# Performance work log

Hardware: AMD Instinct MI355X
Metric: run time of the kernel (lower is better)

## Reference

```python
import jax, jax.numpy as jnp
import numpy as np

N, T, GX, GY, GQ = 16, 64, 256, 256, 256   # solutions, timesteps, source grid, query grid
H, D = 4, 8                                 # attention heads / head dim
SIGMA = 0.2
LY_MIN, LY_MAX = 30.0, 120.0
CU_REF, NI_REF = 0.0029, 0.0018
LX = 100.0


def setup_inputs() -> dict:
    key = jax.random.key(0)
    ks = jax.random.split(key, 7)
    lys = jax.random.uniform(ks[0], (N,), minval=40.0, maxval=110.0)
    ccu = jax.random.uniform(ks[1], (N,), minval=0.001, maxval=CU_REF)
    cni = jax.random.uniform(ks[2], (N,), minval=0.0005, maxval=NI_REF)
    params = jnp.stack([lys, ccu, cni], axis=1).astype(jnp.float32)  # [N,3] raw (Ly, C_Cu, C_Ni)
    x_grids = jnp.tile(jnp.linspace(0.0, LX, GX, dtype=jnp.float32)[None], (N, 1))      # [N,GX]
    y_grids = lys[:, None] * jnp.linspace(0.0, 1.0, GY, dtype=jnp.float32)[None]        # [N,GY]
    c1_src = jax.random.normal(ks[3], (N, T, GX, GY), dtype=jnp.float32)
    c2_src = jax.random.normal(ks[4], (N, T, GX, GY), dtype=jnp.float32)
    Wq_w = 0.1 * jax.random.normal(ks[5], (H * D, 3), dtype=jnp.float32)
    Wk_w = 0.1 * jax.random.normal(ks[6], (H * D, 3), dtype=jnp.float32)
    Wq_b = jnp.zeros((H * D,), jnp.float32)
    Wk_b = jnp.zeros((H * D,), jnp.float32)
    return dict(c1_src=c1_src, c2_src=c2_src, x_grids=x_grids, y_grids=y_grids,
                params=params, Wq_w=Wq_w, Wq_b=Wq_b, Wk_w=Wk_w, Wk_b=Wk_b,
                ly_target=jnp.float32(75.0), c_cu_target=jnp.float32(0.0029),
                c_ni_target=jnp.float32(0.0018))


def _bilinear(c, xg, yg, qx, qy):
    """Linear interp on rectilinear grid, fill_value=0 out of bounds.
    c: [T,Gx,Gy], xg: [Gx], yg: [Gy], qx/qy: [P] -> [T,P]."""
    ix = jnp.clip(jnp.searchsorted(xg, qx, side='right') - 1, 0, xg.shape[0] - 2)
    iy = jnp.clip(jnp.searchsorted(yg, qy, side='right') - 1, 0, yg.shape[0] - 2)
    x0, x1 = xg[ix], xg[ix + 1]
    y0, y1 = yg[iy], yg[iy + 1]
    fx = (qx - x0) / (x1 - x0)
    fy = (qy - y0) / (y1 - y0)
    c00 = c[:, ix, iy]
    c10 = c[:, ix + 1, iy]
    c01 = c[:, ix, iy + 1]
    c11 = c[:, ix + 1, iy + 1]
    v = ((1 - fx) * (1 - fy)) * c00 + (fx * (1 - fy)) * c10 \
        + ((1 - fx) * fy) * c01 + (fx * fy) * c11
    inb = (qx >= xg[0]) & (qx <= xg[-1]) & (qy >= yg[0]) & (qy <= yg[-1])
    return jnp.where(inb[None, :], v, 0.0)


def _forward(c1_src, c2_src, x_grids, y_grids, params, Wq_w, Wq_b, Wk_w, Wk_b,
             ly_target, c_cu_target, c_ni_target):
    # --- parameter normalization (same constants as original) ---
    p = jnp.stack([(params[:, 0] - LY_MIN) / (LY_MAX - LY_MIN),
                   params[:, 1] / CU_REF,
                   params[:, 2] / NI_REF], axis=1)                     # [N,3]
    tgt = jnp.stack([(ly_target - LY_MIN) / (LY_MAX - LY_MIN),
                     c_cu_target / CU_REF,
                     c_ni_target / NI_REF])[None, :]                   # [1,3]
    # --- tiny multi-head attention weights ---
    q = (tgt @ Wq_w.T + Wq_b).reshape(1, H, D)
    k = (p @ Wk_w.T + Wk_b).reshape(p.shape[0], H, D)
    attn = jnp.einsum('nhd,mhd->nmh', k, q) / np.sqrt(D).astype(np.float32)  # [N,1,H]
    attn_w = jax.nn.softmax(attn, axis=0).mean(axis=2).squeeze(1)            # [N]
    # --- gaussian spatial weights ---
    sw = jnp.exp(-0.5 * jnp.sum(((p - tgt) / SIGMA) ** 2, axis=1))
    sw = sw / sw.sum()
    w = attn_w * sw
    w = w / w.sum()
    w = jax.lax.stop_gradient(w)  # original detaches weights before interpolation
    # --- batched bilinear interpolation onto target grid ---
    Lx = x_grids[0, -1]
    unit = jnp.linspace(0.0, 1.0, GQ, dtype=jnp.float32)
    X, Y = jnp.meshgrid(unit * Lx, unit * ly_target, indexing='ij')    # [GQ,GQ]
    qx, qy = X.ravel(), Y.ravel()                                      # [P]
    ys = y_grids * (ly_target / params[:, 0])[:, None]                 # per-solution rescaled Y grids
    interp = jax.vmap(_bilinear, in_axes=(0, 0, 0, None, None))        # -> [N,T,P]
    c1 = jnp.einsum('n,ntp->tp', w, interp(c1_src, x_grids, ys, qx, qy)).reshape(T, GQ, GQ)
    c2 = jnp.einsum('n,ntp->tp', w, interp(c2_src, x_grids, ys, qx, qy)).reshape(T, GQ, GQ)
    # --- boundary conditions ---
    c1 = c1.at[:, :, 0].set(c_cu_target)
    c2 = c2.at[:, :, -1].set(c_ni_target)
    return jnp.stack([c1, c2]), w


def reference(c1_src, c2_src, x_grids, y_grids, params, Wq_w, Wq_b, Wk_w, Wk_b,
              ly_target, c_cu_target, c_ni_target):
    return _forward(c1_src, c2_src, x_grids, y_grids, params, Wq_w, Wq_b, Wk_w, Wk_b,
                    ly_target, c_cu_target, c_ni_target)
```

## Files before the change

kernel.cpp:

```cpp
#include <hip/hip_runtime.h>

#define N_SRC 16
#define T_DIM 64
#define GXD 256
#define GYD 256
#define GQD 256
#define HN 4
#define DN 8
#define TI 16
#define MAXROWS 18
#define OUT_C_ELEMS (2 * T_DIM * GQD * GQD)

#define WS_IY   0
#define WS_WY0  16384
#define WS_WY1  32768
#define WS_IX   49152
#define WS_WX0  50176
#define WS_WX1  51200

__device__ __forceinline__ float unitv(int i) {
    return (i == GQD - 1) ? 1.0f : (float)i * (1.0f / 255.0f);
}

__global__ __launch_bounds__(256) void table_kernel(
    const float* __restrict__ xg, const float* __restrict__ yg,
    const float* __restrict__ params,
    const float* __restrict__ Wq_w, const float* __restrict__ Wq_b,
    const float* __restrict__ Wk_w, const float* __restrict__ Wk_b,
    const float* __restrict__ lyt_p, const float* __restrict__ ccut_p,
    const float* __restrict__ cnit_p,
    float* __restrict__ out_w, char* __restrict__ ws)
{
    __shared__ float xg_sm[GXD];
    __shared__ float ys_sm[N_SRC][GYD];
    __shared__ float w_sm[N_SRC];

    const int tid = threadIdx.x;
    const float lyt = *lyt_p;

    xg_sm[tid] = xg[tid];
    #pragma unroll
    for (int n = 0; n < N_SRC; ++n) {
        float s = lyt / params[n * 3 + 0];
        ys_sm[n][tid] = yg[n * GYD + tid] * s;
    }

    if (tid == 0) {
        const float ccut = *ccut_p, cnit = *cnit_p;
        float tgt[3];
        tgt[0] = (lyt - 30.0f) / 90.0f;
        tgt[1] = ccut / 0.0029f;
        tgt[2] = cnit / 0.0018f;
        float q[HN * DN];
        for (int hd = 0; hd < HN * DN; ++hd)
            q[hd] = tgt[0] * Wq_w[hd * 3 + 0] + tgt[1] * Wq_w[hd * 3 + 1] + tgt[2] * Wq_w[hd * 3 + 2] + Wq_b[hd];
        float p[N_SRC][3];
        float attn[N_SRC][HN];
        for (int n = 0; n < N_SRC; ++n) {
            p[n][0] = (params[n * 3 + 0] - 30.0f) / 90.0f;
            p[n][1] = params[n * 3 + 1] / 0.0029f;
            p[n][2] = params[n * 3 + 2] / 0.0018f;
            for (int h = 0; h < HN; ++h) {
                float acc = 0.0f;
                for (int d = 0; d < DN; ++d) {
                    int hd = h * DN + d;
                    float kv = p[n][0] * Wk_w[hd * 3 + 0] + p[n][1] * Wk_w[hd * 3 + 1] + p[n][2] * Wk_w[hd * 3 + 2] + Wk_b[hd];
                    acc += kv * q[hd];
                }
                attn[n][h] = acc / sqrtf(8.0f);
            }
        }
        float aw[N_SRC];
        for (int n = 0; n < N_SRC; ++n) aw[n] = 0.0f;
        for (int h = 0; h < HN; ++h) {
            float m = attn[0][h];
            for (int n = 1; n < N_SRC; ++n) m = fmaxf(m, attn[n][h]);
            float e[N_SRC], s = 0.0f;
            for (int n = 0; n < N_SRC; ++n) { e[n] = expf(attn[n][h] - m); s += e[n]; }
            for (int n = 0; n < N_SRC; ++n) aw[n] += e[n] / s;
        }
        for (int n = 0; n < N_SRC; ++n) aw[n] *= (1.0f / (float)HN);
        float sw[N_SRC], ss = 0.0f;
        for (int n = 0; n < N_SRC; ++n) {
            float d0 = (p[n][0] - tgt[0]) / 0.2f;
            float d1 = (p[n][1] - tgt[1]) / 0.2f;
            float d2 = (p[n][2] - tgt[2]) / 0.2f;
            sw[n] = expf(-0.5f * (d0 * d0 + d1 * d1 + d2 * d2));
            ss += sw[n];
        }
        float w[N_SRC], wsum = 0.0f;
        for (int n = 0; n < N_SRC; ++n) { w[n] = aw[n] * (sw[n] / ss); wsum += w[n]; }
        for (int n = 0; n < N_SRC; ++n) {
            float wf = w[n] / wsum;
            w_sm[n] = wf;
            out_w[n] = wf;
        }
    }
    __syncthreads();

    int*   iy_tab  = (int*)  (ws + WS_IY);
    float* wy0_tab = (float*)(ws + WS_WY0);
    float* wy1_tab = (float*)(ws + WS_WY1);
    int*   ix_tab  = (int*)  (ws + WS_IX);
    float* wx0_tab = (float*)(ws + WS_WX0);
    float* wx1_tab = (float*)(ws + WS_WX1);

    const int j = tid;
    const float qy = unitv(j) * lyt;
    #pragma unroll
    for (int n = 0; n < N_SRC; ++n) {
        int lo = 0, hi = GYD;
        while (lo < hi) { int mid = (lo + hi) >> 1; if (ys_sm[n][mid] <= qy) lo = mid + 1; else hi = mid; }
        int idx = lo - 1;
        idx = idx < 0 ? 0 : (idx > GYD - 2 ? GYD - 2 : idx);
        float y0 = ys_sm[n][idx], y1 = ys_sm[n][idx + 1];
        float fy = (qy - y0) / (y1 - y0);
        float vy = (qy >= ys_sm[n][0] && qy <= ys_sm[n][GYD - 1]) ? 1.0f : 0.0f;
        float wn = w_sm[n] * vy;
        iy_tab [n * GQD + j] = idx;
        wy0_tab[n * GQD + j] = wn * (1.0f - fy);
        wy1_tab[n * GQD + j] = wn * fy;
    }

    const float Lx = xg_sm[GXD - 1];
    const float qx = unitv(tid) * Lx;
    int lo = 0, hi = GXD;
    while (lo < hi) { int mid = (lo + hi) >> 1; if (xg_sm[mid] <= qx) lo = mid + 1; else hi = mid; }
    int ixi = lo - 1;
    ixi = ixi < 0 ? 0 : (ixi > GXD - 2 ? GXD - 2 : ixi);
    const float x0 = xg_sm[ixi], x1 = xg_sm[ixi + 1];
    const float fx = (qx - x0) / (x1 - x0);
    const float vx = (qx >= xg_sm[0] && qx <= xg_sm[GXD - 1]) ? 1.0f : 0.0f;
    ix_tab [tid] = ixi;
    wx0_tab[tid] = vx * (1.0f - fx);
    wx1_tab[tid] = vx * fx;
}

__device__ __forceinline__ void gl_lds16(const float4* g, float4* l) {
    __builtin_amdgcn_global_load_lds(
        (const __attribute__((address_space(1))) void*)g,
        (__attribute__((address_space(3))) void*)l, 16, 0, 0);
}

__global__ __launch_bounds__(256) void fused_kernel(
    const float* __restrict__ c1, const float* __restrict__ c2,
    const float* __restrict__ ccut_p, const float* __restrict__ cnit_p,
    const char* __restrict__ ws, float* __restrict__ out)
{
    __shared__ float buf[2][MAXROWS * GYD];
    __shared__ int   ixb_sm[TI];
    __shared__ float wx0_sm[TI], wx1_sm[TI];

    const int tid = threadIdx.x;
    const int j = tid;
    const int i0 = blockIdx.x * TI;
    const int t = blockIdx.y;

    const int*   iy_tab  = (const int*)  (ws + WS_IY);
    const float* wy0_tab = (const float*)(ws + WS_WY0);
    const float* wy1_tab = (const float*)(ws + WS_WY1);

    if (tid < TI) {
        ixb_sm[tid] = ((const int*)  (ws + WS_IX)) [i0 + tid];
        wx0_sm[tid] = ((const float*)(ws + WS_WX0))[i0 + tid];
        wx1_sm[tid] = ((const float*)(ws + WS_WX1))[i0 + tid];
    }
    __syncthreads();

    const int x0r = ixb_sm[0];
    int nrows = ixb_sm[TI - 1] + 2 - x0r;
    nrows = nrows > MAXROWS ? MAXROWS : nrows;
    const int chunks4 = nrows * (GYD / 4);

    int   r0r[TI];
    float wx0r[TI], wx1r[TI];
    #pragma unroll
    for (int ii = 0; ii < TI; ++ii) {
        r0r[ii]  = ixb_sm[ii] - x0r;
        wx0r[ii] = wx0_sm[ii];
        wx1r[ii] = wx1_sm[ii];
    }

    float acc1[TI], acc2[TI];
    #pragma unroll
    for (int ii = 0; ii < TI; ++ii) { acc1[ii] = 0.0f; acc2[ii] = 0.0f; }

    auto plane_src = [&](int p) -> const float4* {
        const int n = p >> 1;
        const float* base = (p & 1) ? c2 : c1;
        return (const float4*)(base + (((size_t)n * T_DIM + t) * GXD + x0r) * GYD);
    };

    {
        const float4* g = plane_src(0);
        float4* l = (float4*)&buf[0][0];
        #pragma unroll
        for (int k = 0; k < 5; ++k) {
            int c = tid + k * 256;
            if (c < chunks4) gl_lds16(g + c, l + c);
        }
    }

    int   iyv = 0;
    float wy0v = 0.0f, wy1v = 0.0f;

    for (int p = 0; p < 2 * N_SRC; ++p) {
        __builtin_amdgcn_s_waitcnt(0);
        __syncthreads();

        if (p + 1 < 2 * N_SRC) {
            const float4* g = plane_src(p + 1);
            float4* l = (float4*)&buf[(p + 1) & 1][0];
            #pragma unroll
            for (int k = 0; k < 5; ++k) {
                int c = tid + k * 256;
                if (c < chunks4) gl_lds16(g + c, l + c);
            }
        }

        const int n = p >> 1;
        if ((p & 1) == 0) {
            iyv  = iy_tab [n * GQD + j];
            wy0v = wy0_tab[n * GQD + j];
            wy1v = wy1_tab[n * GQD + j];
        }

        const float* B = &buf[p & 1][0];
        int loaded = -1;
        float vm1 = 0.0f, vcur = 0.0f;
        if ((p & 1) == 0) {
            #pragma unroll
            for (int ii = 0; ii < TI; ++ii) {
                const int r1 = r0r[ii] + 1;
                while (loaded < r1) {
                    ++loaded;
                    vm1 = vcur;
                    vcur = wy0v * B[loaded * GYD + iyv] + wy1v * B[loaded * GYD + iyv + 1];
                }
                acc1[ii] += wx0r[ii] * vm1 + wx1r[ii] * vcur;
            }
        } else {
            #pragma unroll
            for (int ii = 0; ii < TI; ++ii) {
                const int r1 = r0r[ii] + 1;
                while (loaded < r1) {
                    ++loaded;
                    vm1 = vcur;
                    vcur = wy0v * B[loaded * GYD + iyv] + wy1v * B[loaded * GYD + iyv + 1];
                }
                acc2[ii] += wx0r[ii] * vm1 + wx1r[ii] * vcur;
            }
        }
    }

    const float ccut = *ccut_p, cnit = *cnit_p;
    #pragma unroll
    for (int ii = 0; ii < TI; ++ii) {
        const int i = i0 + ii;
        float o1 = acc1[ii];
        float o2 = acc2[ii];
        if (j == 0)       o1 = ccut;
        if (j == GQD - 1) o2 = cnit;
        out[(t * GQD + i) * GQD + j] = o1;
        out[((T_DIM + t) * GQD + i) * GQD + j] = o2;
    }
}

extern "C" void kernel_launch(void* const* d_in, const int* in_sizes, int n_in,
                              void* d_out, int out_size, void* d_ws, size_t ws_size,
                              hipStream_t stream) {
    const float* c1     = (const float*)d_in[0];
    const float* c2     = (const float*)d_in[1];
    const float* xg     = (const float*)d_in[2];
    const float* yg     = (const float*)d_in[3];
    const float* params = (const float*)d_in[4];
    const float* Wq_w   = (const float*)d_in[5];
    const float* Wq_b   = (const float*)d_in[6];
    const float* Wk_w   = (const float*)d_in[7];
    const float* Wk_b   = (const float*)d_in[8];
    const float* lyt    = (const float*)d_in[9];
    const float* ccut   = (const float*)d_in[10];
    const float* cnit   = (const float*)d_in[11];
    float* out = (float*)d_out;
    float* out_w = out + OUT_C_ELEMS;
    char* ws = (char*)d_ws;

    table_kernel<<<1, 256, 0, stream>>>(xg, yg, params, Wq_w, Wq_b, Wk_w, Wk_b,
                                        lyt, ccut, cnit, out_w, ws);
    dim3 grid(GQD / TI, T_DIM);
    fused_kernel<<<grid, 256, 0, stream>>>(c1, c2, ccut, cnit, ws, out);
}
```

Measured before the change: 629.9 us.

## Replace LDS double-buffered staging with direct global gathers and smaller row tiles

Drops the async global-to-LDS double-buffered copy of each source plane's row band and instead gathers the four bilinear corners straight from global memory through the cache. The per-block row tile is halved, launch bounds ask for 4 blocks per CU, and output writes become nontemporal stores. This removes the per-plane barriers, the LDS footprint and the redundant staging of whole rows. In exchange, adjacent query rows re-read shared source rows through L1/L2 rather than LDS, and per-thread scattered loads replace coalesced bulk copies.

```diff
diff --git a/kernel.cpp b/kernel.cpp
--- a/kernel.cpp
+++ b/kernel.cpp
@@ -7,8 +7,7 @@
 #define GQD 256
 #define HN 4
 #define DN 8
-#define TI 16
-#define MAXROWS 18
+#define TI 8
 #define OUT_C_ELEMS (2 * T_DIM * GQD * GQD)
 
 #define WS_IY   0
@@ -136,18 +135,11 @@
     wx1_tab[tid] = vx * fx;
 }
 
-__device__ __forceinline__ void gl_lds16(const float4* g, float4* l) {
-    __builtin_amdgcn_global_load_lds(
-        (const __attribute__((address_space(1))) void*)g,
-        (__attribute__((address_space(3))) void*)l, 16, 0, 0);
-}
-
-__global__ __launch_bounds__(256) void fused_kernel(
+__global__ __launch_bounds__(256, 4) void fused_kernel(
     const float* __restrict__ c1, const float* __restrict__ c2,
     const float* __restrict__ ccut_p, const float* __restrict__ cnit_p,
     const char* __restrict__ ws, float* __restrict__ out)
 {
-    __shared__ float buf[2][MAXROWS * GYD];
     __shared__ int   ixb_sm[TI];
     __shared__ float wx0_sm[TI], wx1_sm[TI];
 
@@ -167,16 +159,11 @@
     }
     __syncthreads();
 
-    const int x0r = ixb_sm[0];
-    int nrows = ixb_sm[TI - 1] + 2 - x0r;
-    nrows = nrows > MAXROWS ? MAXROWS : nrows;
-    const int chunks4 = nrows * (GYD / 4);
-
-    int   r0r[TI];
+    int   rq  [TI];
     float wx0r[TI], wx1r[TI];
     #pragma unroll
     for (int ii = 0; ii < TI; ++ii) {
-        r0r[ii]  = ixb_sm[ii] - x0r;
+        rq  [ii] = ixb_sm[ii] * GYD;
         wx0r[ii] = wx0_sm[ii];
         wx1r[ii] = wx1_sm[ii];
     }
@@ -185,71 +172,34 @@
     #pragma unroll
     for (int ii = 0; ii < TI; ++ii) { acc1[ii] = 0.0f; acc2[ii] = 0.0f; }
 
-    auto plane_src = [&](int p) -> const float4* {
-        const int n = p >> 1;
-        const float* base = (p & 1) ? c2 : c1;
-        return (const float4*)(base + (((size_t)n * T_DIM + t) * GXD + x0r) * GYD);
-    };
-
-    {
-        const float4* g = plane_src(0);
-        float4* l = (float4*)&buf[0][0];
+    const size_t tbase = (size_t)t * (GXD * GYD);
+    const float* b1 = c1 + tbase;
+    const float* b2 = c2 + tbase;
+
+    #pragma unroll 4
+    for (int n = 0; n < N_SRC; ++n) {
+        const int   iy  = iy_tab [n * GQD + j];
+        const float wy0 = wy0_tab[n * GQD + j];
+        const float wy1 = wy1_tab[n * GQD + j];
+        const float* p1 = b1 + (size_t)n * ((size_t)T_DIM * GXD * GYD);
+        const float* p2 = b2 + (size_t)n * ((size_t)T_DIM * GXD * GYD);
         #pragma unroll
-        for (int k = 0; k < 5; ++k) {
-            int c = tid + k * 256;
-            if (c < chunks4) gl_lds16(g + c, l + c);
-        }
-    }
-
-    int   iyv = 0;
-    float wy0v = 0.0f, wy1v = 0.0f;
-
-    for (int p = 0; p < 2 * N_SRC; ++p) {
-        __builtin_amdgcn_s_waitcnt(0);
-        __syncthreads();
-
-        if (p + 1 < 2 * N_SRC) {
-            const float4* g = plane_src(p + 1);
-            float4* l = (float4*)&buf[(p + 1) & 1][0];
-            #pragma unroll
-            for (int k = 0; k < 5; ++k) {
-                int c = tid + k * 256;
-                if (c < chunks4) gl_lds16(g + c, l + c);
-            }
-        }
-
-        const int n = p >> 1;
-        if ((p & 1) == 0) {
-            iyv  = iy_tab [n * GQD + j];
-            wy0v = wy0_tab[n * GQD + j];
-            wy1v = wy1_tab[n * GQD + j];
-        }
-
-        const float* B = &buf[p & 1][0];
-        int loaded = -1;
-        float vm1 = 0.0f, vcur = 0.0f;
-        if ((p & 1) == 0) {
-            #pragma unroll
-            for (int ii = 0; ii < TI; ++ii) {
-                const int r1 = r0r[ii] + 1;
-                while (loaded < r1) {
-                    ++loaded;
-                    vm1 = vcur;
-                    vcur = wy0v * B[loaded * GYD + iyv] + wy1v * B[loaded * GYD + iyv + 1];
-                }
-                acc1[ii] += wx0r[ii] * vm1 + wx1r[ii] * vcur;
-            }
-        } else {
-            #pragma unroll
-            for (int ii = 0; ii < TI; ++ii) {
-                const int r1 = r0r[ii] + 1;
-                while (loaded < r1) {
-                    ++loaded;
-                    vm1 = vcur;
-                    vcur = wy0v * B[loaded * GYD + iyv] + wy1v * B[loaded * GYD + iyv + 1];
-                }
-                acc2[ii] += wx0r[ii] * vm1 + wx1r[ii] * vcur;
-            }
+        for (int ii = 0; ii < TI; ++ii) {
+            const int o = rq[ii] + iy;
+            const float a00 = p1[o];
+            const float a01 = p1[o + 1];
+            const float a10 = p1[o + GYD];
+            const float a11 = p1[o + GYD + 1];
+            const float b00 = p2[o];
+            const float b01 = p2[o + 1];
+            const float b10 = p2[o + GYD];
+            const float b11 = p2[o + GYD + 1];
+            const float v0 = wy0 * a00 + wy1 * a01;
+            const float v1 = wy0 * a10 + wy1 * a11;
+            acc1[ii] += wx0r[ii] * v0 + wx1r[ii] * v1;
+            const float u0 = wy0 * b00 + wy1 * b01;
+            const float u1 = wy0 * b10 + wy1 * b11;
+            acc2[ii] += wx0r[ii] * u0 + wx1r[ii] * u1;
         }
     }
 
@@ -261,8 +211,8 @@
         float o2 = acc2[ii];
         if (j == 0)       o1 = ccut;
         if (j == GQD - 1) o2 = cnit;
-        out[(t * GQD + i) * GQD + j] = o1;
-        out[((T_DIM + t) * GQD + i) * GQD + j] = o2;
+        __builtin_nontemporal_store(o1, &out[((size_t)t * GQD + i) * GQD + j]);
+        __builtin_nontemporal_store(o2, &out[(((size_t)T_DIM + t) * GQD + i) * GQD + j]);
     }
 }
 
```

Measured after the change: 646.2 us. 1.03x slower.
